# Kernel tuning notes

Hardware: AMD Instinct MI355X
Metric: run time of the kernel (lower is better)

Reference implementation:

```python
import jax, jax.numpy as jnp
import numpy as np

N_POINTS = 65536      # total nodes across the batch
NDIMS = 3
NUM_THETAS = 64       # directions
BUMP_STEPS = 32       # discretization steps of [-radius, radius]
NUM_GRAPHS = 64       # number of point clouds in the batch
RADIUS = 1.1
SCALE = 100.0         # sigmoid sharpness


def setup_inputs() -> dict:
    key = jax.random.key(0)
    k1, k2, k3 = jax.random.split(key, 3)
    x = jax.random.normal(k1, (N_POINTS, NDIMS), dtype=jnp.float32)
    # unit-norm direction vectors on the sphere, columns of v: [ndims, num_thetas]
    v = jax.random.normal(k2, (NDIMS, NUM_THETAS), dtype=jnp.float32)
    v = v / jnp.linalg.norm(v, axis=0, keepdims=True)
    # lin = discretization of [-radius, radius], matches nn.Parameter linspace
    lin = jnp.linspace(-RADIUS, RADIUS, BUMP_STEPS, dtype=jnp.float32)
    # sorted batch index assigning each node to a graph (torch_geometric convention)
    batch = jnp.sort(jax.random.randint(k3, (N_POINTS,), 0, NUM_GRAPHS, dtype=jnp.int32))
    return {"x": x, "v": v, "lin": lin, "batch": batch}


def reference(x, v, lin, batch):
    # node heights: inner product of coordinates with each direction -> [N, T]
    nh = x @ v
    # broadcast soft-threshold: sigmoid(scale * (lin - nh)) -> [N, S, T]
    # (torch builds [S,1,N,T] then movedims to [N,1,S,T]; same values)
    ecc = jax.nn.sigmoid(SCALE * (lin[None, :, None] - nh[:, None, :]))
    # segment scatter-add over nodes per graph -> [B, S, T]
    ect = jax.ops.segment_sum(ecc, batch, num_segments=NUM_GRAPHS)
    return ect  # torch output after .squeeze(): [batch, bump_steps, num_thetas]
```

## Files before the change

kernel.cpp:

```cpp
#include <hip/hip_runtime.h>

#define T        64
#define S        32
#define CHUNK    32
#define SPT      8

__global__ __launch_bounds__(256, 8) void ect_kernel(
    const float* __restrict__ x, const float* __restrict__ v,
    const float* __restrict__ lin, const int* __restrict__ batch,
    float* __restrict__ out, int n_points)
{
    __shared__ float sx[CHUNK * 3];
    __shared__ int   sb[CHUNK];

    const int tid = threadIdx.x;
    const int t   = tid & 63;
    const int s0  = (tid >> 6) * SPT;

    const float K = 144.26950408889634f;

    const float v0 = v[0 * T + t];
    const float v1 = v[1 * T + t];
    const float v2 = v[2 * T + t];

    const float c0 = lin[s0] * K;
    const float m  = __builtin_amdgcn_exp2f((lin[0] - lin[1]) * K);

    const int base = blockIdx.x * CHUNK;
    const int rem  = min(CHUNK, n_points - base);

    if (rem == CHUNK) {
        if (tid < CHUNK * 3 / 4) ((float4*)sx)[tid] = ((const float4*)(x + base * 3))[tid];
        if (tid < CHUNK)         sb[tid] = batch[base + tid];
    } else {
        for (int i = tid; i < rem * 3; i += 256) sx[i] = x[base * 3 + i];
        for (int i = tid; i < rem;     i += 256) sb[i] = batch[base + i];
    }
    __syncthreads();

    float acc[SPT];
#pragma unroll
    for (int j = 0; j < SPT; j++) acc[j] = 0.0f;

    int cur = sb[0];
#pragma unroll 2
    for (int n = 0; n < rem; n++) {
        const int b = sb[n];
        if (b != cur) {
            float* o = out + (cur * S + s0) * T + t;
#pragma unroll
            for (int j = 0; j < SPT; j++) {
                atomicAdd(o + j * T, acc[j]);
                acc[j] = 0.0f;
            }
            cur = b;
        }
        const float nh = sx[n * 3 + 0] * v0 + sx[n * 3 + 1] * v1 + sx[n * 3 + 2] * v2;
        float e = __builtin_amdgcn_exp2f(nh * K - c0);
#pragma unroll
        for (int j = 0; j < SPT; j++) {
            acc[j] += __builtin_amdgcn_rcpf(1.0f + e);
            e *= m;
        }
    }
    float* o = out + (cur * S + s0) * T + t;
#pragma unroll
    for (int j = 0; j < SPT; j++) atomicAdd(o + j * T, acc[j]);
}

extern "C" void kernel_launch(void* const* d_in, const int* in_sizes, int n_in,
                              void* d_out, int out_size, void* d_ws, size_t ws_size,
                              hipStream_t stream) {
    const float* x     = (const float*)d_in[0];
    const float* v     = (const float*)d_in[1];
    const float* lin   = (const float*)d_in[2];
    const int*   batch = (const int*)d_in[3];
    float* out = (float*)d_out;

    const int n_points = in_sizes[0] / 3;
    const int blocks   = (n_points + CHUNK - 1) / CHUNK;

    hipMemsetAsync(d_out, 0, (size_t)out_size * sizeof(float), stream);
    ect_kernel<<<blocks, 256, 0, stream>>>(x, v, lin, batch, out, n_points);
}
```

Baseline: 82.03 us.

## Truncate sigmoid sum to three nearest bins plus prefix-sum histogram

Each point's sigmoid curve over the 32 bins is split into three exactly evaluated bins around the crossing point. The bins beyond them count as saturated 1s, recorded in an LDS histogram and recovered with a per-direction prefix sum. Per-graph segments inside a 64-point chunk are found with a ballot, and results go out through LDS atomics and then global atomics. This cuts transcendental work from 32 to 3 evaluations per point and direction. In exchange it adds LDS atomic traffic, extra barriers per segment, and a small truncation error from treating far bins as exactly 0 or 1.

Result: slower. 146.8 us (+79.0%).

```diff
diff --git a/kernel.cpp b/kernel.cpp
--- a/kernel.cpp
+++ b/kernel.cpp
@@ -1,71 +1,90 @@
 #include <hip/hip_runtime.h>
 
-#define T        64
-#define S        32
-#define CHUNK    32
-#define SPT      8
+#define T      64
+#define S      32
+#define CHUNK  64
+#define NW     4
 
-__global__ __launch_bounds__(256, 8) void ect_kernel(
+__global__ __launch_bounds__(256, 4) void ect_kernel(
     const float* __restrict__ x, const float* __restrict__ v,
     const float* __restrict__ lin, const int* __restrict__ batch,
     float* __restrict__ out, int n_points)
 {
-    __shared__ float sx[CHUNK * 3];
-    __shared__ int   sb[CHUNK];
+    __shared__ float acc[T * 33];
+    __shared__ float hist[T * 33];
+    __shared__ float tot[T * 5];
 
     const int tid = threadIdx.x;
     const int t   = tid & 63;
-    const int s0  = (tid >> 6) * SPT;
+    const int w   = tid >> 6;
 
-    const float K = 144.26950408889634f;
+    const float lin0     = lin[0];
+    const float step     = lin[1] - lin0;
+    const float inv_step = 1.0f / step;
+    const float K2 = (100.0f * step) * 1.4426950408889634f;
+    const float r  = __builtin_amdgcn_exp2f(-K2);
 
     const float v0 = v[0 * T + t];
     const float v1 = v[1 * T + t];
     const float v2 = v[2 * T + t];
 
-    const float c0 = lin[s0] * K;
-    const float m  = __builtin_amdgcn_exp2f((lin[0] - lin[1]) * K);
+    const int base    = blockIdx.x * CHUNK;
+    const int rem     = min(CHUNK, n_points - base);
+    const int accbase = t * 33;
 
-    const int base = blockIdx.x * CHUNK;
-    const int rem  = min(CHUNK, n_points - base);
+    int seg_start = 0;
+    while (seg_start < rem) {
+        for (int i = tid; i < T * 33; i += 256) { acc[i] = 0.0f; hist[i] = 0.0f; }
+        __syncthreads();
 
-    if (rem == CHUNK) {
-        if (tid < CHUNK * 3 / 4) ((float4*)sx)[tid] = ((const float4*)(x + base * 3))[tid];
-        if (tid < CHUNK)         sb[tid] = batch[base + tid];
-    } else {
-        for (int i = tid; i < rem * 3; i += 256) sx[i] = x[base * 3 + i];
-        for (int i = tid; i < rem;     i += 256) sb[i] = batch[base + i];
+        const int g = batch[base + seg_start];
+        const bool bd = (t < rem) && (t > seg_start) && (batch[base + t] != g);
+        const unsigned long long mask = __ballot(bd);
+        const int seg_end = mask ? (int)__builtin_ctzll(mask) : rem;
+
+#pragma unroll 2
+        for (int n = seg_start + w; n < seg_end; n += NW) {
+            const float* xp = x + 3 * (base + n);
+            const float nh = xp[0] * v0 + xp[1] * v1 + xp[2] * v2;
+            const float f  = (nh - lin0) * inv_step;
+            const float fs = ceilf(f);
+            const int   ss = (int)fs;
+            const float gg = fs - f;
+            float e = __builtin_amdgcn_exp2f(K2 * (1.0f - gg));
+#pragma unroll
+            for (int j = 0; j < 3; j++) {
+                const int   s   = ss - 1 + j;
+                const float sig = __builtin_amdgcn_rcpf(1.0f + e);
+                const bool  ok  = ((unsigned)s < 32u);
+                const int   col = ok ? s : 32;
+                const float val = ok ? sig : 0.0f;
+                atomicAdd(&acc[accbase + col], val);
+                e *= r;
+            }
+            const int c = min(max(ss + 2, 0), 32);
+            atomicAdd(&hist[accbase + c], 1.0f);
+        }
+        __syncthreads();
+
+        float h[8], sumA = 0.0f;
+#pragma unroll
+        for (int j = 0; j < 8; j++) { h[j] = hist[accbase + 8 * w + j]; sumA += h[j]; }
+        tot[t * 5 + w] = sumA;
+        __syncthreads();
+
+        float run = 0.0f;
+        for (int q = 0; q < w; q++) run += tot[t * 5 + q];
+        float* outg = out + (g * S) * T + t;
+#pragma unroll
+        for (int j = 0; j < 8; j++) {
+            run += h[j];
+            const int   s = 8 * w + j;
+            const float valout = acc[accbase + s] + run;
+            if (valout != 0.0f) atomicAdd(&outg[s * T], valout);
+        }
+        __syncthreads();
+        seg_start = seg_end;
     }
-    __syncthreads();
-
-    float acc[SPT];
-#pragma unroll
-    for (int j = 0; j < SPT; j++) acc[j] = 0.0f;
-
-    int cur = sb[0];
-#pragma unroll 2
-    for (int n = 0; n < rem; n++) {
-        const int b = sb[n];
-        if (b != cur) {
-            float* o = out + (cur * S + s0) * T + t;
-#pragma unroll
-            for (int j = 0; j < SPT; j++) {
-                atomicAdd(o + j * T, acc[j]);
-                acc[j] = 0.0f;
-            }
-            cur = b;
-        }
-        const float nh = sx[n * 3 + 0] * v0 + sx[n * 3 + 1] * v1 + sx[n * 3 + 2] * v2;
-        float e = __builtin_amdgcn_exp2f(nh * K - c0);
-#pragma unroll
-        for (int j = 0; j < SPT; j++) {
-            acc[j] += __builtin_amdgcn_rcpf(1.0f + e);
-            e *= m;
-        }
-    }
-    float* o = out + (cur * S + s0) * T + t;
-#pragma unroll
-    for (int j = 0; j < SPT; j++) atomicAdd(o + j * T, acc[j]);
 }
 
 extern "C" void kernel_launch(void* const* d_in, const int* in_sizes, int n_in,
```
